# Kernel optimization log

Measured on AMD Instinct MI355X. Metric: run time of the kernel, lower is better.

The kernel has to match this reference:

```python
import jax, jax.numpy as jnp
import numpy as np

B, N, DIM = 32, 577, 768   # N = num_patches + 1
H, DH = 12, 64             # heads, dim_head; inner_dim = H*DH = 768
NEG = -987654321.0         # LSA diagonal mask value from the source


def setup_inputs() -> dict:
    key = jax.random.key(0)
    ks = jax.random.split(key, 5)
    inner = H * DH
    base_scale = DH ** -0.5
    return {
        "x": jax.random.normal(ks[0], (B, N, DIM), dtype=jnp.float32),
        "W_qkv": jax.random.normal(ks[1], (DIM, inner * 3), dtype=jnp.float32) * (DIM ** -0.5),
        "scale": base_scale * (1.0 + 0.01 * jax.random.normal(ks[2], (H,), dtype=jnp.float32)),
        "W_out": jax.random.normal(ks[3], (inner, DIM), dtype=jnp.float32) * (inner ** -0.5),
        "b_out": jnp.zeros((DIM,), dtype=jnp.float32),
    }


def reference(x, W_qkv, scale, W_out, b_out):
    b, n, _ = x.shape
    qkv = x @ W_qkv                                   # [b, n, 3*H*DH]
    q, k, v = jnp.split(qkv, 3, axis=-1)
    to_heads = lambda t: t.reshape(b, n, H, DH).transpose(0, 2, 1, 3)  # b h n d
    q, k, v = to_heads(q), to_heads(k), to_heads(v)
    # per-head learnable scale (LSA)
    dots = jnp.einsum('bhid,bhjd->bhij', q, k) * scale[None, :, None, None]
    # mask self-attention diagonal (eye scatter in the torch source)
    eye = jnp.eye(n, dtype=bool)
    dots = jnp.where(eye[None, None], NEG, dots)
    attn = jax.nn.softmax(dots, axis=-1)
    out = jnp.einsum('bhij,bhjd->bhid', attn, v)      # b h n d
    out = out.transpose(0, 2, 1, 3).reshape(b, n, H * DH)
    return out @ W_out + b_out
```

## Files before the change

### kernel.cpp

```cpp
#include <hip/hip_runtime.h>


typedef _Float16 half8  __attribute__((ext_vector_type(8)));
typedef _Float16 h4f    __attribute__((ext_vector_type(4)));
typedef __fp16   hv2    __attribute__((ext_vector_type(2)));
typedef __fp16   hv4    __attribute__((ext_vector_type(4)));
typedef float    floatx4 __attribute__((ext_vector_type(4)));

#define MTOT   18464
#define NEG_V  (-987654321.0f)
#define VTS    584

__device__ __forceinline__ void gl_lds16(const _Float16* g, _Float16* l) {
    __builtin_amdgcn_global_load_lds(
        (const __attribute__((address_space(1))) unsigned int*)g,
        (__attribute__((address_space(3))) unsigned int*)l,
        16, 0, 0);
}

__global__ __launch_bounds__(256) void cvt_x(const float* __restrict__ x,
                                             _Float16* __restrict__ x16) {
    const size_t idx = ((size_t)blockIdx.x * 256 + threadIdx.x) * 8;
    half8 h = {};
    if (idx < (size_t)MTOT * 768) {
        float4 a = *(const float4*)(x + idx);
        float4 b = *(const float4*)(x + idx + 4);
        h[0] = (_Float16)a.x; h[1] = (_Float16)a.y;
        h[2] = (_Float16)a.z; h[3] = (_Float16)a.w;
        h[4] = (_Float16)b.x; h[5] = (_Float16)b.y;
        h[6] = (_Float16)b.z; h[7] = (_Float16)b.w;
    }
    *(half8*)(x16 + idx) = h;
}

__global__ __launch_bounds__(256) void transpose_both(const float* __restrict__ Wqkv,
                                                      const float* __restrict__ Wout,
                                                      _Float16* __restrict__ WqkvT,
                                                      _Float16* __restrict__ WoutT) {
    const float* src;
    _Float16* dst;
    int Ncol, k0, n0;
    if (blockIdx.y < 24) {
        src = Wqkv; dst = WqkvT; Ncol = 2304;
        k0 = blockIdx.y * 32; n0 = blockIdx.x * 32;
    } else {
        if (blockIdx.x >= 24) return;
        src = Wout; dst = WoutT; Ncol = 768;
        k0 = (blockIdx.y - 24) * 32; n0 = blockIdx.x * 32;
    }
    __shared__ float tile[32][33];
    const int tx = threadIdx.x & 31, ty = threadIdx.x >> 5;
    for (int i = 0; i < 32; i += 8)
        tile[ty + i][tx] = src[(size_t)(k0 + ty + i) * Ncol + (n0 + tx)];
    __syncthreads();
    for (int i = 0; i < 32; i += 8)
        dst[(size_t)(n0 + ty + i) * 768 + (k0 + tx)] = (_Float16)tile[tx][ty + i];
}

__global__ __launch_bounds__(256, 4) void gemm_qkv(const _Float16* __restrict__ x16,
                                                   const _Float16* __restrict__ wT,
                                                   const float* __restrict__ scale,
                                                   _Float16* __restrict__ qg,
                                                   _Float16* __restrict__ kg,
                                                   _Float16* __restrict__ vT) {
    __shared__ _Float16 As[2][128 * 32];
    __shared__ _Float16 Bs[2][128 * 32];
    const unsigned orig = blockIdx.x;
    const unsigned xcd = orig & 7u, bidx = orig >> 3;
    const unsigned swz = (xcd < 2u ? xcd * 327u : 654u + (xcd - 2u) * 326u) + bidx;
    const unsigned mi = swz / 18u, ni = swz - mi * 18u;
    const int m0 = (int)mi * 128, n0 = (int)ni * 128;
    const int tid = threadIdx.x;
    const int lane = tid & 63, wv = tid >> 6;
    const int wrow = wv >> 1, wcol = wv & 1;
    const int lr = lane & 15, lq = lane >> 4;

    const int r1 = tid >> 2,        c1 = (((tid & 3) ^ ((r1 >> 1) & 3)) * 8);
    const int r2 = 64 + (tid >> 2), c2 = (((tid & 3) ^ ((r2 >> 1) & 3)) * 8);
    const int xc = (lq ^ ((lr >> 1) & 3)) * 8;

    floatx4 acc[4][4];
    const floatx4 fz = {0.f, 0.f, 0.f, 0.f};
    for (int i = 0; i < 4; ++i)
        for (int j = 0; j < 4; ++j) acc[i][j] = fz;

    #define STAGE_QKV(ki, bfx)                                                      \
        do {                                                                        \
            const int kk_ = (ki) * 32;                                              \
            gl_lds16(x16 + (size_t)(m0 + r1) * 768 + kk_ + c1, &As[bfx][wv*64*8]);  \
            gl_lds16(x16 + (size_t)(m0 + r2) * 768 + kk_ + c2,                      \
                     &As[bfx][(256 + wv*64) * 8]);                                  \
            gl_lds16(wT + (size_t)(n0 + r1) * 768 + kk_ + c1, &Bs[bfx][wv*64*8]);   \
            gl_lds16(wT + (size_t)(n0 + r2) * 768 + kk_ + c2,                       \
                     &Bs[bfx][(256 + wv*64) * 8]);                                  \
        } while (0)

    STAGE_QKV(0, 0);
    for (int ki = 0; ki < 24; ++ki) {
        const int bf = ki & 1;
        if (ki < 23) {
            STAGE_QKV(ki + 1, bf ^ 1);
            asm volatile("s_waitcnt vmcnt(4)" ::: "memory");
        } else {
            asm volatile("s_waitcnt vmcnt(0)" ::: "memory");
        }
        asm volatile("s_barrier" ::: "memory");

        half8 af[4], bfr[4];
        #pragma unroll
        for (int i = 0; i < 4; ++i)
            af[i] = *(const half8*)&As[bf][(wrow * 64 + i * 16 + lr) * 32 + xc];
        #pragma unroll
        for (int j = 0; j < 4; ++j)
            bfr[j] = *(const half8*)&Bs[bf][(wcol * 64 + j * 16 + lr) * 32 + xc];
        #pragma unroll
        for (int i = 0; i < 4; ++i)
            #pragma unroll
            for (int j = 0; j < 4; ++j)
                acc[i][j] = __builtin_amdgcn_mfma_f32_16x16x32_f16(af[i], bfr[j], acc[i][j], 0, 0, 0);

        asm volatile("s_waitcnt lgkmcnt(0)\n\ts_barrier" ::: "memory");
    }
    #undef STAGE_QKV

    const int cbase = n0 + wcol * 64;
    const int which = cbase / 768;
    const int h = (cbase - which * 768) >> 6;
    const float qsc = (which == 0) ? scale[h] * 1.4426950408889634f : 1.0f;
    #pragma unroll
    for (int j = 0; j < 4; ++j) {
        const int d = j * 16 + lr;
        #pragma unroll
        for (int i = 0; i < 4; ++i)
            #pragma unroll
            for (int r = 0; r < 4; ++r) {
                const int row = m0 + wrow * 64 + i * 16 + lq * 4 + r;
                if (row >= MTOT) continue;
                const unsigned bb = (unsigned)row / 577u;
                const unsigned nn = (unsigned)row - bb * 577u;
                const _Float16 val = (_Float16)(acc[i][j][r] * qsc);
                const size_t head = (size_t)(bb * 12 + h);
                if (which == 0)      qg[(head * 577 + nn) * 64 + d] = val;
                else if (which == 1) kg[(head * 577 + nn) * 64 + d] = val;
                else                 vT[(head * 64 + d) * VTS + nn] = val;
            }
    }
}

__global__ __launch_bounds__(256) void attn_kernel(const _Float16* __restrict__ qg,
                                                   const _Float16* __restrict__ kg,
                                                   const _Float16* __restrict__ vT,
                                                   _Float16* __restrict__ Og) {
    __shared__ __align__(16) _Float16 Ks[2][64 * 64];
    __shared__ __align__(16) _Float16 Vs[2][64 * 64];
    const unsigned orig = blockIdx.x;
    const unsigned swz = (orig & 7u) * 240u + (orig >> 3);
    const int qt = (int)(swz % 5u);
    const unsigned hb = swz / 5u;
    const int h = (int)(hb % 12u), b = (int)(hb / 12u);
    const int tid = threadIdx.x, lane = tid & 63, wv = tid >> 6;
    const int lr = lane & 15, lq = lane >> 4;
    const size_t head = (size_t)(b * 12 + h);
    const _Float16* qh = qg + head * 577 * 64;
    const _Float16* kh = kg + head * 577 * 64;
    const _Float16* vh = vT + head * 64 * VTS;
    const int q0 = qt * 128;
    const int xs = lq ^ (lr & 7), xs4 = xs ^ 4;

    half8 bq[2][2];
    #pragma unroll
    for (int st = 0; st < 2; ++st) {
        const int qi = q0 + st * 64 + wv * 16 + lr;
        const int qc = qi < 577 ? qi : 576;
        bq[st][0] = *(const half8*)(qh + (size_t)qc * 64 + lq * 8);
        bq[st][1] = *(const half8*)(qh + (size_t)qc * 64 + 32 + lq * 8);
    }

    #define PREF(kt_, pb_)                                               \
        do {                                                             \
            const int j0_ = (kt_) * 64;                                  \
            {   const int c_ = wv * 64 + lane;                           \
                const int r_ = c_ >> 3, cl_ = (c_ & 7) ^ (r_ & 7);       \
                gl_lds16(kh + (size_t)(j0_ + r_) * 64 + cl_ * 8,         \
                         &Ks[pb_][(wv * 64) * 8]);                       \
                gl_lds16(vh + (size_t)r_ * VTS + j0_ + cl_ * 8,          \
                         &Vs[pb_][(wv * 64) * 8]);   }                   \
            {   const int c_ = 256 + wv * 64 + lane;                     \
                const int r_ = c_ >> 3, cl_ = (c_ & 7) ^ (r_ & 7);       \
                gl_lds16(kh + (size_t)(j0_ + r_) * 64 + cl_ * 8,         \
                         &Ks[pb_][(256 + wv * 64) * 8]);                 \
                gl_lds16(vh + (size_t)r_ * VTS + j0_ + cl_ * 8,          \
                         &Vs[pb_][(256 + wv * 64) * 8]);   }             \
        } while (0)

    const floatx4 fz = {0.f, 0.f, 0.f, 0.f};
    floatx4 ot[2][4];
    #pragma unroll
    for (int st = 0; st < 2; ++st)
        #pragma unroll
        for (int c = 0; c < 4; ++c) ot[st][c] = fz;
    float sacc[2] = {0.f, 0.f};

    PREF(0, 0);
    for (int kt = 0; kt < 10; ++kt) {
        const int bf = kt & 1;
        if (kt < 9) {
            PREF(kt + 1, bf ^ 1);
            asm volatile("s_waitcnt vmcnt(4)" ::: "memory");
        } else {
            asm volatile("s_waitcnt vmcnt(0)" ::: "memory");
        }
        asm volatile("s_barrier" ::: "memory");

        half8 ak[4][2];
        #pragma unroll
        for (int ct = 0; ct < 4; ++ct) {
            const int base = (ct * 16 + lr) * 64;
            ak[ct][0] = *(const half8*)&Ks[bf][base + xs * 8];
            ak[ct][1] = *(const half8*)&Ks[bf][base + xs4 * 8];
        }

        floatx4 s[2][4];
        #pragma unroll
        for (int st = 0; st < 2; ++st)
            #pragma unroll
            for (int ct = 0; ct < 4; ++ct) {
                floatx4 t = __builtin_amdgcn_mfma_f32_16x16x32_f16(ak[ct][0], bq[st][0], fz, 0, 0, 0);
                s[st][ct] = __builtin_amdgcn_mfma_f32_16x16x32_f16(ak[ct][1], bq[st][1], t, 0, 0, 0);
            }

        if (kt == 9) {
            #pragma unroll
            for (int st = 0; st < 2; ++st) {
                s[st][0][0] = (lq == 0) ? s[st][0][0] : -INFINITY;
                s[st][0][1] = -INFINITY; s[st][0][2] = -INFINITY; s[st][0][3] = -INFINITY;
                #pragma unroll
                for (int ct = 1; ct < 4; ++ct) {
                    s[st][ct][0] = -INFINITY; s[st][ct][1] = -INFINITY;
                    s[st][ct][2] = -INFINITY; s[st][ct][3] = -INFINITY;
                }
            }
        }
        #pragma unroll
        for (int st = 0; st < 2; ++st) {
            if (kt == qt * 2 + st) {
                #pragma unroll
                for (int ct = 0; ct < 4; ++ct)
                    if (ct == wv) {
                        #pragma unroll
                        for (int r = 0; r < 4; ++r)
                            if (lq * 4 + r == lr) s[st][ct][r] = -INFINITY;
                    }
            }
        }

        hv4 pk[2][4];
        #pragma unroll
        for (int st = 0; st < 2; ++st)
            #pragma unroll
            for (int ct = 0; ct < 4; ++ct) {
                const float p0 = __builtin_amdgcn_exp2f(s[st][ct][0]);
                const float p1 = __builtin_amdgcn_exp2f(s[st][ct][1]);
                const float p2 = __builtin_amdgcn_exp2f(s[st][ct][2]);
                const float p3 = __builtin_amdgcn_exp2f(s[st][ct][3]);
                sacc[st] += (p0 + p1) + (p2 + p3);
                const hv2 lo = __builtin_amdgcn_cvt_pkrtz(p0, p1);
                const hv2 hi = __builtin_amdgcn_cvt_pkrtz(p2, p3);
                pk[st][ct] = __builtin_shufflevector(lo, hi, 0, 1, 2, 3);
            }

        #pragma unroll
        for (int jc = 0; jc < 4; ++jc) {
            const int csv = ((jc << 1) | (lq >> 1)) ^ (lr & 7);
            #pragma unroll
            for (int ctd = 0; ctd < 4; ++ctd) {
                const hv4 av = *(const hv4*)&Vs[bf][(ctd * 16 + lr) * 64 + csv * 8 + (lq & 1) * 4];
                #pragma unroll
                for (int st = 0; st < 2; ++st)
                    ot[st][ctd] = __builtin_amdgcn_mfma_f32_16x16x16f16(av, pk[st][jc], ot[st][ctd], 0, 0, 0);
            }
        }

        asm volatile("s_waitcnt lgkmcnt(0)\n\ts_barrier" ::: "memory");
    }
    #undef PREF

    #pragma unroll
    for (int st = 0; st < 2; ++st) {
        float l = sacc[st];
        l += __shfl_xor(l, 16, 64);
        l += __shfl_xor(l, 32, 64);
        const float linv = 1.f / l;
        const int i = q0 + st * 64 + wv * 16 + lr;
        if (i < 577) {
            #pragma unroll
            for (int ctd = 0; ctd < 4; ++ctd) {
                h4f ov;
                #pragma unroll
                for (int r = 0; r < 4; ++r) ov[r] = (_Float16)(ot[st][ctd][r] * linv);
                *(h4f*)(Og + ((size_t)(b * 577 + i)) * 768 + h * 64 + ctd * 16 + lq * 4) = ov;
            }
        }
    }
}

__global__ __launch_bounds__(256, 4) void gemm_out(const _Float16* __restrict__ Og,
                                                   const _Float16* __restrict__ wT,
                                                   const float* __restrict__ bias,
                                                   float* __restrict__ out) {
    __shared__ _Float16 As[2][128 * 32];
    __shared__ _Float16 Bs[2][128 * 32];
    const unsigned orig = blockIdx.x;
    const unsigned xcd = orig & 7u, bidx = orig >> 3;
    const unsigned swz = (xcd < 6u ? xcd * 109u : 654u + (xcd - 6u) * 108u) + bidx;
    const unsigned mi = swz / 6u, ni = swz - mi * 6u;
    const int m0 = (int)mi * 128, n0 = (int)ni * 128;
    const int tid = threadIdx.x;
    const int lane = tid & 63, wv = tid >> 6;
    const int wrow = wv >> 1, wcol = wv & 1;
    const int lr = lane & 15, lq = lane >> 4;

    const int r1 = tid >> 2,        c1 = (((tid & 3) ^ ((r1 >> 1) & 3)) * 8);
    const int r2 = 64 + (tid >> 2), c2 = (((tid & 3) ^ ((r2 >> 1) & 3)) * 8);
    const int xc = (lq ^ ((lr >> 1) & 3)) * 8;

    floatx4 acc[4][4];
    const floatx4 fz = {0.f, 0.f, 0.f, 0.f};
    for (int i = 0; i < 4; ++i)
        for (int j = 0; j < 4; ++j) acc[i][j] = fz;

    #define STAGE_OUT(ki, bfx)                                                      \
        do {                                                                        \
            const int kk_ = (ki) * 32;                                              \
            gl_lds16(Og + (size_t)(m0 + r1) * 768 + kk_ + c1, &As[bfx][wv*64*8]);   \
            gl_lds16(Og + (size_t)(m0 + r2) * 768 + kk_ + c2,                       \
                     &As[bfx][(256 + wv*64) * 8]);                                  \
            gl_lds16(wT + (size_t)(n0 + r1) * 768 + kk_ + c1, &Bs[bfx][wv*64*8]);   \
            gl_lds16(wT + (size_t)(n0 + r2) * 768 + kk_ + c2,                       \
                     &Bs[bfx][(256 + wv*64) * 8]);                                  \
        } while (0)

    STAGE_OUT(0, 0);
    for (int ki = 0; ki < 24; ++ki) {
        const int bf = ki & 1;
        if (ki < 23) {
            STAGE_OUT(ki + 1, bf ^ 1);
            asm volatile("s_waitcnt vmcnt(4)" ::: "memory");
        } else {
            asm volatile("s_waitcnt vmcnt(0)" ::: "memory");
        }
        asm volatile("s_barrier" ::: "memory");

        half8 af[4], bfr[4];
        #pragma unroll
        for (int i = 0; i < 4; ++i)
            af[i] = *(const half8*)&As[bf][(wrow * 64 + i * 16 + lr) * 32 + xc];
        #pragma unroll
        for (int j = 0; j < 4; ++j)
            bfr[j] = *(const half8*)&Bs[bf][(wcol * 64 + j * 16 + lr) * 32 + xc];
        #pragma unroll
        for (int i = 0; i < 4; ++i)
            #pragma unroll
            for (int j = 0; j < 4; ++j)
                acc[i][j] = __builtin_amdgcn_mfma_f32_16x16x32_f16(af[i], bfr[j], acc[i][j], 0, 0, 0);

        asm volatile("s_waitcnt lgkmcnt(0)\n\ts_barrier" ::: "memory");
    }
    #undef STAGE_OUT

    #pragma unroll
    for (int j = 0; j < 4; ++j) {
        const int c = n0 + wcol * 64 + j * 16 + lr;
        const float bv = bias[c];
        #pragma unroll
        for (int i = 0; i < 4; ++i)
            #pragma unroll
            for (int r = 0; r < 4; ++r) {
                const int row = m0 + wrow * 64 + i * 16 + lq * 4 + r;
                if (row < MTOT) out[(size_t)row * 768 + c] = acc[i][j][r] + bv;
            }
    }
}

extern "C" void kernel_launch(void* const* d_in, const int* in_sizes, int n_in,
                              void* d_out, int out_size, void* d_ws, size_t ws_size,
                              hipStream_t stream) {
    const float* x      = (const float*)d_in[0];
    const float* W_qkv  = (const float*)d_in[1];
    const float* scale  = (const float*)d_in[2];
    const float* W_out  = (const float*)d_in[3];
    const float* b_out  = (const float*)d_in[4];
    float* out = (float*)d_out;

    char* ws = (char*)d_ws;
    _Float16* x16   = (_Float16*)(ws);
    _Float16* Og    = x16;
    _Float16* qg    = (_Float16*)(ws + 28508160u);
    _Float16* kg    = (_Float16*)(ws + 28508160u + 28360704u);
    _Float16* vT    = (_Float16*)(ws + 28508160u + 2u * 28360704u);
    _Float16* WqkvT = (_Float16*)(ws + 28508160u + 2u * 28360704u + 28704768u);
    _Float16* WoutT = WqkvT + (size_t)2304 * 768;

    cvt_x<<<6960, 256, 0, stream>>>(x, x16);
    transpose_both<<<dim3(72, 48), 256, 0, stream>>>(W_qkv, W_out, WqkvT, WoutT);
    gemm_qkv<<<2610, 256, 0, stream>>>(x16, WqkvT, scale, qg, kg, vT);
    attn_kernel<<<1920, 256, 0, stream>>>(qg, kg, vT, Og);
    gemm_out<<<870, 256, 0, stream>>>(Og, WoutT, b_out, out);
}
```

Before: 341.9 us.

## Merge prep kernels and stage V-transpose epilogue through LDS for vector stores

Fuses the x conversion and weight transpose kernels into one launch, removing a kernel launch and the gap between them. In the QKV GEMM, the V-part epilogue now writes accumulators into a swizzled LDS tile, shares one LDS array for A and B, and then emits 16-byte contiguous stores along the sequence dimension into vT, where before it issued scattered 2-byte strided stores. Rows near batch boundaries or the end of M fall back to per-element stores. This adds an extra barrier and LDS round trip on V blocks.

```diff
diff --git a/kernel.cpp b/kernel.cpp
--- a/kernel.cpp
+++ b/kernel.cpp
@@ -18,37 +18,40 @@
         16, 0, 0);
 }
 
-__global__ __launch_bounds__(256) void cvt_x(const float* __restrict__ x,
-                                             _Float16* __restrict__ x16) {
-    const size_t idx = ((size_t)blockIdx.x * 256 + threadIdx.x) * 8;
-    half8 h = {};
-    if (idx < (size_t)MTOT * 768) {
-        float4 a = *(const float4*)(x + idx);
-        float4 b = *(const float4*)(x + idx + 4);
-        h[0] = (_Float16)a.x; h[1] = (_Float16)a.y;
-        h[2] = (_Float16)a.z; h[3] = (_Float16)a.w;
-        h[4] = (_Float16)b.x; h[5] = (_Float16)b.y;
-        h[6] = (_Float16)b.z; h[7] = (_Float16)b.w;
-    }
-    *(half8*)(x16 + idx) = h;
-}
-
-__global__ __launch_bounds__(256) void transpose_both(const float* __restrict__ Wqkv,
-                                                      const float* __restrict__ Wout,
-                                                      _Float16* __restrict__ WqkvT,
-                                                      _Float16* __restrict__ WoutT) {
+__global__ __launch_bounds__(256) void prep(const float* __restrict__ x,
+                                            _Float16* __restrict__ x16,
+                                            const float* __restrict__ Wqkv,
+                                            const float* __restrict__ Wout,
+                                            _Float16* __restrict__ WqkvT,
+                                            _Float16* __restrict__ WoutT) {
+    __shared__ float tile[32][33];
+    if (blockIdx.x < 6960u) {
+        const size_t idx = ((size_t)blockIdx.x * 256 + threadIdx.x) * 8;
+        half8 h = {};
+        if (idx < (size_t)MTOT * 768) {
+            float4 a = *(const float4*)(x + idx);
+            float4 b = *(const float4*)(x + idx + 4);
+            h[0] = (_Float16)a.x; h[1] = (_Float16)a.y;
+            h[2] = (_Float16)a.z; h[3] = (_Float16)a.w;
+            h[4] = (_Float16)b.x; h[5] = (_Float16)b.y;
+            h[6] = (_Float16)b.z; h[7] = (_Float16)b.w;
+        }
+        *(half8*)(x16 + idx) = h;
+        return;
+    }
+    const unsigned tb = blockIdx.x - 6960u;
+    const int bx = (int)(tb % 72u), by = (int)(tb / 72u);
     const float* src;
     _Float16* dst;
     int Ncol, k0, n0;
-    if (blockIdx.y < 24) {
+    if (by < 24) {
         src = Wqkv; dst = WqkvT; Ncol = 2304;
-        k0 = blockIdx.y * 32; n0 = blockIdx.x * 32;
+        k0 = by * 32; n0 = bx * 32;
     } else {
-        if (blockIdx.x >= 24) return;
+        if (bx >= 24) return;
         src = Wout; dst = WoutT; Ncol = 768;
-        k0 = (blockIdx.y - 24) * 32; n0 = blockIdx.x * 32;
-    }
-    __shared__ float tile[32][33];
+        k0 = (by - 24) * 32; n0 = bx * 32;
+    }
     const int tx = threadIdx.x & 31, ty = threadIdx.x >> 5;
     for (int i = 0; i < 32; i += 8)
         tile[ty + i][tx] = src[(size_t)(k0 + ty + i) * Ncol + (n0 + tx)];
@@ -63,8 +66,7 @@
                                                    _Float16* __restrict__ qg,
                                                    _Float16* __restrict__ kg,
                                                    _Float16* __restrict__ vT) {
-    __shared__ _Float16 As[2][128 * 32];
-    __shared__ _Float16 Bs[2][128 * 32];
+    __shared__ _Float16 As[4][128 * 32];
     const unsigned orig = blockIdx.x;
     const unsigned xcd = orig & 7u, bidx = orig >> 3;
     const unsigned swz = (xcd < 2u ? xcd * 327u : 654u + (xcd - 2u) * 326u) + bidx;
@@ -90,9 +92,10 @@
             gl_lds16(x16 + (size_t)(m0 + r1) * 768 + kk_ + c1, &As[bfx][wv*64*8]);  \
             gl_lds16(x16 + (size_t)(m0 + r2) * 768 + kk_ + c2,                      \
                      &As[bfx][(256 + wv*64) * 8]);                                  \
-            gl_lds16(wT + (size_t)(n0 + r1) * 768 + kk_ + c1, &Bs[bfx][wv*64*8]);   \
+            gl_lds16(wT + (size_t)(n0 + r1) * 768 + kk_ + c1,                       \
+                     &As[2 + (bfx)][wv*64*8]);                                      \
             gl_lds16(wT + (size_t)(n0 + r2) * 768 + kk_ + c2,                       \
-                     &Bs[bfx][(256 + wv*64) * 8]);                                  \
+                     &As[2 + (bfx)][(256 + wv*64) * 8]);                            \
         } while (0)
 
     STAGE_QKV(0, 0);
@@ -112,7 +115,7 @@
             af[i] = *(const half8*)&As[bf][(wrow * 64 + i * 16 + lr) * 32 + xc];
         #pragma unroll
         for (int j = 0; j < 4; ++j)
-            bfr[j] = *(const half8*)&Bs[bf][(wcol * 64 + j * 16 + lr) * 32 + xc];
+            bfr[j] = *(const half8*)&As[2 + bf][(wcol * 64 + j * 16 + lr) * 32 + xc];
         #pragma unroll
         for (int i = 0; i < 4; ++i)
             #pragma unroll
@@ -125,6 +128,52 @@
 
     const int cbase = n0 + wcol * 64;
     const int which = cbase / 768;
+
+    if (which == 2) {
+        _Float16* ep = &As[0][0];
+        #pragma unroll
+        for (int j = 0; j < 4; ++j) {
+            const int dg = wcol * 64 + j * 16 + lr;
+            #pragma unroll
+            for (int i = 0; i < 4; ++i)
+                #pragma unroll
+                for (int r = 0; r < 4; ++r) {
+                    const int ml = wrow * 64 + i * 16 + lq * 4 + r;
+                    const int col = ((((ml >> 3) ^ (dg & 7)) << 3) | (ml & 7));
+                    ep[dg * 128 + col] = (_Float16)acc[i][j][r];
+                }
+        }
+        __syncthreads();
+        const int h0 = (n0 - 1536) >> 6;
+        const int dg = tid >> 1;
+        const int h = h0 + (dg >> 6);
+        _Float16* dstrow = vT + ((size_t)0);
+        #pragma unroll
+        for (int c = 0; c < 8; ++c) {
+            const int mc = ((tid & 1) << 3) | c;
+            const int m = m0 + (mc << 3);
+            if (m >= MTOT) continue;
+            half8 v = *(const half8*)&ep[dg * 128 + ((mc ^ (dg & 7)) << 3)];
+            const unsigned bb = (unsigned)m / 577u;
+            const unsigned nn = (unsigned)m - bb * 577u;
+            if (nn <= 569u && m + 7 < MTOT) {
+                _Float16* dst = vT + ((size_t)(bb * 12 + h) * 64 + (dg & 63)) * VTS + nn;
+                __builtin_memcpy(dst, &v, 16);
+            } else {
+                #pragma unroll
+                for (int e = 0; e < 8; ++e) {
+                    const int mm = m + e;
+                    if (mm >= MTOT) break;
+                    const unsigned bbe = (unsigned)mm / 577u;
+                    const unsigned nne = (unsigned)mm - bbe * 577u;
+                    vT[((size_t)(bbe * 12 + h) * 64 + (dg & 63)) * VTS + nne] = v[e];
+                }
+            }
+        }
+        (void)dstrow;
+        return;
+    }
+
     const int h = (cbase - which * 768) >> 6;
     const float qsc = (which == 0) ? scale[h] * 1.4426950408889634f : 1.0f;
     #pragma unroll
@@ -141,8 +190,7 @@
                 const _Float16 val = (_Float16)(acc[i][j][r] * qsc);
                 const size_t head = (size_t)(bb * 12 + h);
                 if (which == 0)      qg[(head * 577 + nn) * 64 + d] = val;
-                else if (which == 1) kg[(head * 577 + nn) * 64 + d] = val;
-                else                 vT[(head * 64 + d) * VTS + nn] = val;
+                else                 kg[(head * 577 + nn) * 64 + d] = val;
             }
     }
 }
@@ -401,8 +449,7 @@
     _Float16* WqkvT = (_Float16*)(ws + 28508160u + 2u * 28360704u + 28704768u);
     _Float16* WoutT = WqkvT + (size_t)2304 * 768;
 
-    cvt_x<<<6960, 256, 0, stream>>>(x, x16);
-    transpose_both<<<dim3(72, 48), 256, 0, stream>>>(W_qkv, W_out, WqkvT, WoutT);
+    prep<<<10416, 256, 0, stream>>>(x, x16, W_qkv, W_out, WqkvT, WoutT);
     gemm_qkv<<<2610, 256, 0, stream>>>(x16, WqkvT, scale, qg, kg, vT);
     attn_kernel<<<1920, 256, 0, stream>>>(qg, kg, vT, Og);
     gemm_out<<<870, 256, 0, stream>>>(Og, WoutT, b_out, out);
```

New measurement: 322.3 us. 5.7% less time.
